# Kernel optimization log

Measured on AMD Instinct MI355X. Metric: run time of the kernel, lower is better.

The kernel has to match this reference:

```python
import jax, jax.numpy as jnp
import numpy as np

B = 512
N_ENT = 100000
N_REL = 64
D = 200          # embed_dim
D1 = 10          # embed_shape (emb_dim1)
D2 = 20          # embed_dim // embed_shape (emb_dim2)
K = 3            # kernel_size
C = 32           # out_channels
FC_IN = C * (2 * D1 - K + 1) * (D2 - K + 1)  # 32*18*18 = 10368
EPS = 1e-5       # BatchNorm eps
LS = 0.1         # label_smoothing
LAM = 1e-5       # kg_l2_loss_lambda


def setup_inputs() -> dict:
    key = jax.random.key(0)
    ks = jax.random.split(key, 8)
    return dict(
        entity_w=jax.random.normal(ks[0], (N_ENT, D), jnp.float32) * 0.1,
        relation_w=jax.random.normal(ks[1], (N_REL, D), jnp.float32) * 0.1,
        conv_w=jax.random.normal(ks[2], (C, 1, K, K), jnp.float32) * 0.1,
        conv_b=jnp.zeros((C,), jnp.float32),
        fc_w=jax.random.normal(ks[3], (D, FC_IN), jnp.float32) * 0.02,
        fc_b=jnp.zeros((D,), jnp.float32),
        b=jnp.zeros((N_ENT,), jnp.float32),
        bn0_g=jnp.ones((1,), jnp.float32), bn0_b=jnp.zeros((1,), jnp.float32),
        bn1_g=jnp.ones((C,), jnp.float32), bn1_b=jnp.zeros((C,), jnp.float32),
        bn2_g=jnp.ones((D,), jnp.float32), bn2_b=jnp.zeros((D,), jnp.float32),
        h=jax.random.randint(ks[4], (B,), 0, N_ENT),
        r=jax.random.randint(ks[5], (B,), 0, N_REL),
        pos_t=jax.random.randint(ks[6], (B,), 0, N_ENT),
    )


def _bn(x, g, b, axes, shape):
    # training-mode batchnorm (batch statistics), biased variance as in torch
    m = jnp.mean(x, axes, keepdims=True)
    v = jnp.var(x, axes, keepdims=True)
    return (x - m) * jax.lax.rsqrt(v + EPS) * g.reshape(shape) + b.reshape(shape)


def _l2_mean(x):
    # torch: mean(sum(x**2, dim=1) / 2)
    return jnp.mean(jnp.sum(x * x, axis=1) / 2.0)


def reference(entity_w, relation_w, conv_w, conv_b, fc_w, fc_b, b,
              bn0_g, bn0_b, bn1_g, bn1_b, bn2_g, bn2_b, h, r, pos_t):
    h_e = entity_w[h].reshape(B, 1, D1, D2)
    r_e = relation_w[r].reshape(B, 1, D1, D2)
    x = jnp.concatenate([h_e, r_e], axis=2)           # [B,1,2*D1,D2]
    x = _bn(x, bn0_g, bn0_b, (0, 2, 3), (1, 1, 1, 1))
    x = jax.lax.conv_general_dilated(
        x, conv_w, (1, 1), 'VALID',
        dimension_numbers=('NCHW', 'OIHW', 'NCHW')) + conv_b.reshape(1, C, 1, 1)
    x = _bn(x, bn1_g, bn1_b, (0, 2, 3), (1, C, 1, 1))
    x = jax.nn.relu(x).reshape(B, -1)                 # [B, FC_IN]
    x = x @ fc_w.T + fc_b                             # [B, D]
    x = _bn(x, bn2_g, bn2_b, (0,), (1, D))
    x = jax.nn.leaky_relu(x)                          # slope 0.01 = torch default
    scores = x @ entity_w.T + b                       # [B, N_ENT]
    # BCEWithLogits with smoothed label y = (1-LS)*onehot(pos_t) + 1/N_ENT,
    # loss = mean(softplus(s) - s*y); one-hot never materialized.
    sp_sum = jnp.sum(jax.nn.softplus(scores))
    xy_sum = jnp.sum(scores) / N_ENT + (1.0 - LS) * jnp.sum(
        scores[jnp.arange(B), pos_t])
    kg_loss = (sp_sum - xy_sum) / (B * N_ENT)
    l2 = _l2_mean(h_e) + _l2_mean(r_e) + _l2_mean(conv_w) + _l2_mean(fc_w)
    return kg_loss + LAM * l2
```

## Files before the change

### kernel.cpp

```cpp
#include <hip/hip_runtime.h>
#include <math.h>

#define NB_B 512
#define NE 100000
#define NE_PAD 100032
#define DD 200
#define CC 32
#define FCIN 10368
#define HW 324
#define BNEPS 1e-5f
#define KP 224

#define ENT_BLKS 10941
#define FCW_BLKS 1013
#define GATH_OFF (ENT_BLKS + FCW_BLKS)

typedef __attribute__((ext_vector_type(8))) short short8;
typedef __attribute__((ext_vector_type(4))) float floatx4;


static __device__ __forceinline__ float blk_reduce(float v, volatile float* sbuf) {
  for (int o = 32; o > 0; o >>= 1) v += __shfl_down(v, o, 64);
  int lane = threadIdx.x & 63, wid = threadIdx.x >> 6;
  if (lane == 0) sbuf[wid] = v;
  __syncthreads();
  float r = 0.f;
  int nw = (blockDim.x + 63) >> 6;
  if ((int)threadIdx.x < nw) r = sbuf[threadIdx.x];
  if (threadIdx.x < 64) {
    for (int o = 32; o > 0; o >>= 1) r += __shfl_down(r, o, 64);
  }
  __syncthreads();
  return r;
}

static __device__ __forceinline__ unsigned short f32_to_bf16(float f) {
  unsigned int u = __float_as_uint(f);
  u += 0x7fffu + ((u >> 16) & 1u);
  return (unsigned short)(u >> 16);
}
static __device__ __forceinline__ float bf16_to_f32(unsigned short b) {
  return __uint_as_float(((unsigned int)b) << 16);
}

__global__ __launch_bounds__(256) void k_cvt(const float* __restrict__ ent,
                                             unsigned short* __restrict__ entb,
                                             const float* __restrict__ fcw,
                                             unsigned short* __restrict__ fcwb,
                                             const float* __restrict__ rel,
                                             const int* __restrict__ h,
                                             const int* __restrict__ r,
                                             float* __restrict__ x0,
                                             double* dacc) {
  if (blockIdx.x < ENT_BLKS) {
    int g = blockIdx.x * 256 + threadIdx.x;
    int row = g / 28;
    int c8 = (g - row * 28) * 8;
    ushort4 o0, o1;
    if (c8 < 200 && row < NE) {
      const float4* s = (const float4*)(ent + (long)row * DD + c8);
      float4 u = s[0], v = s[1];
      o0.x = f32_to_bf16(u.x); o0.y = f32_to_bf16(u.y);
      o0.z = f32_to_bf16(u.z); o0.w = f32_to_bf16(u.w);
      o1.x = f32_to_bf16(v.x); o1.y = f32_to_bf16(v.y);
      o1.z = f32_to_bf16(v.z); o1.w = f32_to_bf16(v.w);
    } else {
      o0.x = o0.y = o0.z = o0.w = 0;
      o1.x = o1.y = o1.z = o1.w = 0;
    }
    ushort4* d = (ushort4*)(entb + (long)row * KP + c8);
    d[0] = o0; d[1] = o1;
  } else if (blockIdx.x < GATH_OFF) {
    int g = (blockIdx.x - ENT_BLKS) * 256 + threadIdx.x;
    float sq = 0.f;
    if (g < 259200) {
      const float4* s = (const float4*)(fcw + (long)g * 8);
      float4 u = s[0], v = s[1];
      sq = u.x*u.x + u.y*u.y + u.z*u.z + u.w*u.w
         + v.x*v.x + v.y*v.y + v.z*v.z + v.w*v.w;
      ushort4 o0, o1;
      o0.x = f32_to_bf16(u.x); o0.y = f32_to_bf16(u.y);
      o0.z = f32_to_bf16(u.z); o0.w = f32_to_bf16(u.w);
      o1.x = f32_to_bf16(v.x); o1.y = f32_to_bf16(v.y);
      o1.z = f32_to_bf16(v.z); o1.w = f32_to_bf16(v.w);
      ushort4* d = (ushort4*)(fcwb + (long)g * 8);
      d[0] = o0; d[1] = o1;
    }
    __shared__ float sbuf[8];
    float tq = blk_reduce(sq, sbuf);
    if (threadIdx.x == 0) atomicAdd(&dacc[67], (double)tq);
  } else {
    int b = blockIdx.x - GATH_OFF;
    int hi = h[b], ri = r[b];
    float s = 0.f, sq = 0.f;
    for (int i = threadIdx.x; i < 400; i += 256) {
      float v = (i < 200) ? ent[(long)hi * DD + i] : rel[(long)ri * DD + (i - 200)];
      x0[b * 400 + i] = v;
      s += v; sq += v * v;
    }
    __shared__ float sbuf[8];
    float ts = blk_reduce(s, sbuf);
    float tq = blk_reduce(sq, sbuf);
    if (threadIdx.x == 0) {
      atomicAdd(&dacc[0], (double)ts);
      atomicAdd(&dacc[1], (double)tq);
    }
  }
}

__global__ __launch_bounds__(256) void k_conv(const float* __restrict__ x0,
                       const float* __restrict__ convw, const float* __restrict__ convb,
                       const float* __restrict__ g0, const float* __restrict__ b0,
                       unsigned short* __restrict__ yb, double* dacc) {
  __shared__ float xs[400], wsm[288], cbs[32], ssum[32], ssq[32];
  __shared__ float a0s, s0s;
  int b = blockIdx.x, t = threadIdx.x;
  for (int i = t; i < 400; i += 256) xs[i] = x0[b * 400 + i];
  for (int i = t; i < 288; i += 256) wsm[i] = convw[i];
  if (t < 32) cbs[t] = convb[t];
  if (t == 0) {
    double m = dacc[0] / 204800.0;
    double v = dacc[1] / 204800.0 - m * m;
    float a = g0[0] * rsqrtf((float)v + BNEPS);
    a0s = a; s0s = b0[0] - (float)m * a;
  }
  __syncthreads();
  float a0 = a0s, s0 = s0s;
  for (int i = t; i < 400; i += 256) xs[i] = a0 * xs[i] + s0;
  __syncthreads();
  int c = t >> 3, sub = t & 7;
  const float* w = &wsm[c * 9];
  float cb = cbs[c];
  float s = 0.f, sq = 0.f;
  for (int e = sub; e < HW; e += 8) {
    int oh = e / 18, ow = e - oh * 18;
    const float* xp = &xs[oh * 20 + ow];
    float acc = cb
       + xp[0] * w[0] + xp[1] * w[1] + xp[2] * w[2]
       + xp[20] * w[3] + xp[21] * w[4] + xp[22] * w[5]
       + xp[40] * w[6] + xp[41] * w[7] + xp[42] * w[8];
    yb[(long)b * FCIN + c * HW + e] = f32_to_bf16(acc);
    s += acc; sq += acc * acc;
  }
  s += __shfl_xor(s, 1, 64); sq += __shfl_xor(sq, 1, 64);
  s += __shfl_xor(s, 2, 64); sq += __shfl_xor(sq, 2, 64);
  s += __shfl_xor(s, 4, 64); sq += __shfl_xor(sq, 4, 64);
  if (sub == 0) { ssum[c] = s; ssq[c] = sq; }
  __syncthreads();
  if (t < 32) {
    atomicAdd(&dacc[2 + t], (double)ssum[t]);
    atomicAdd(&dacc[34 + t], (double)ssq[t]);
  }
}

__global__ __launch_bounds__(256) void k_prep(unsigned short* __restrict__ yb,
                                              const float* __restrict__ g1,
                                              const float* __restrict__ b1,
                                              const double* __restrict__ dacc) {
  __shared__ float a1s[32], sh1s[32];
  int t = threadIdx.x;
  if (t < 32) {
    double cnt = 512.0 * 324.0;
    double m = dacc[2 + t] / cnt, v = dacc[34 + t] / cnt - m * m;
    float a = g1[t] * rsqrtf((float)v + BNEPS);
    a1s[t] = a; sh1s[t] = b1[t] - (float)m * a;
  }
  __syncthreads();
  int g = blockIdx.x * 256 + t;
  int row = g / 1296;
  int c8 = (g - row * 1296) * 8;
  unsigned short* p = yb + (long)row * FCIN + c8;
  ushort4 v0 = ((ushort4*)p)[0], v1 = ((ushort4*)p)[1];
  unsigned short e[8] = {v0.x, v0.y, v0.z, v0.w, v1.x, v1.y, v1.z, v1.w};
#pragma unroll
  for (int j = 0; j < 8; j++) {
    int c = (c8 + j) / HW;
    float f = a1s[c] * bf16_to_f32(e[j]) + sh1s[c];
    e[j] = f32_to_bf16(fmaxf(f, 0.f));
  }
  v0.x = e[0]; v0.y = e[1]; v0.z = e[2]; v0.w = e[3];
  v1.x = e[4]; v1.y = e[5]; v1.z = e[6]; v1.w = e[7];
  ((ushort4*)p)[0] = v0; ((ushort4*)p)[1] = v1;
}

__global__ __launch_bounds__(64) void k_fc3(const unsigned short* __restrict__ yb,
                                            const unsigned short* __restrict__ fcwb,
                                            float* __restrict__ Cp) {
  int wid = blockIdx.x;
  int ks = wid >> 5, rem = wid & 31;
  int mt = rem >> 2, nt = rem & 3;
  int m0 = mt * 64, n0 = nt * 64;
  int lane = threadIdx.x;
  int quad = lane >> 4, lr = lane & 15;
  long kbeg = (long)ks * 864;

  const unsigned short* arow[4];
  const unsigned short* brow[4];
#pragma unroll
  for (int mi = 0; mi < 4; mi++)
    arow[mi] = yb + (long)(m0 + mi * 16 + lr) * FCIN + kbeg + quad * 8;
#pragma unroll
  for (int ni = 0; ni < 4; ni++) {
    int d = n0 + ni * 16 + lr;
    if (d > DD - 1) d = DD - 1;
    brow[ni] = fcwb + (long)d * FCIN + kbeg + quad * 8;
  }

  floatx4 acc[4][4];
#pragma unroll
  for (int i = 0; i < 4; i++)
#pragma unroll
    for (int j = 0; j < 4; j++) acc[i][j] = (floatx4){0.f, 0.f, 0.f, 0.f};

  short8 sA[3][4], sB[3][4];
#pragma unroll
  for (int c = 0; c < 3; c++) {
#pragma unroll
    for (int mi = 0; mi < 4; mi++) sA[c][mi] = *(const short8*)(arow[mi] + c * 32);
#pragma unroll
    for (int ni = 0; ni < 4; ni++) sB[c][ni] = *(const short8*)(brow[ni] + c * 32);
  }
  for (int c3 = 0; c3 < 9; c3++) {
    int cc = c3 * 3;
#pragma unroll
    for (int j = 0; j < 3; j++) {
#pragma unroll
      for (int ni = 0; ni < 4; ni++)
#pragma unroll
        for (int mi = 0; mi < 4; mi++)
          acc[mi][ni] = __builtin_amdgcn_mfma_f32_16x16x32_bf16(sA[j][mi], sB[j][ni], acc[mi][ni], 0, 0, 0);
      int nxt = cc + j + 3;
      if (nxt < 27) {
#pragma unroll
        for (int mi = 0; mi < 4; mi++) sA[j][mi] = *(const short8*)(arow[mi] + nxt * 32);
#pragma unroll
        for (int ni = 0; ni < 4; ni++) sB[j][ni] = *(const short8*)(brow[ni] + nxt * 32);
      }
    }
  }

  float* out = Cp + (long)ks * (NB_B * DD);
#pragma unroll
  for (int ni = 0; ni < 4; ni++) {
    int d = n0 + ni * 16 + lr;
    if (d < DD) {
#pragma unroll
      for (int mi = 0; mi < 4; mi++) {
        int mbase = m0 + mi * 16 + quad * 4;
#pragma unroll
        for (int rg = 0; rg < 4; rg++)
          out[(mbase + rg) * DD + d] = acc[mi][ni][rg];
      }
    }
  }
}

__global__ void k_fcbn(const float* __restrict__ Cp, const float* __restrict__ fcb,
                       const float* __restrict__ g2, const float* __restrict__ b2,
                       float* __restrict__ Cfc, float* __restrict__ a2,
                       float* __restrict__ b2c) {
  int d = blockIdx.x, lane = threadIdx.x;
  float fb = fcb[d];
  float s = 0.f, sq = 0.f;
  for (int b = lane; b < NB_B; b += 64) {
    float v = 0.f;
#pragma unroll
    for (int p = 0; p < 12; p++) v += Cp[(long)p * (NB_B * DD) + b * DD + d];
    Cfc[b * DD + d] = v;
    float w = v + fb;
    s += w; sq += w * w;
  }
  for (int o = 32; o > 0; o >>= 1) { s += __shfl_down(s, o, 64); sq += __shfl_down(sq, o, 64); }
  if (lane == 0) {
    float m = s / 512.f, v = sq / 512.f - m * m;
    float a = g2[d] * rsqrtf(v + BNEPS);
    a2[d] = a; b2c[d] = b2[d] - m * a;
  }
}

__global__ __launch_bounds__(256) void k_xfinal(const float* __restrict__ Cfc,
                         const float* __restrict__ fcb,
                         const float* __restrict__ a2, const float* __restrict__ b2c,
                         const float* __restrict__ ent, const float* __restrict__ bias,
                         const int* __restrict__ pos,
                         float* __restrict__ xf, unsigned short* __restrict__ xfb,
                         double* dacc) {
  __shared__ float xs[224];
  __shared__ float sbuf[8];
  int b = blockIdx.x, t = threadIdx.x;
  if (t < KP) {
    float xv = 0.f;
    if (t < DD) {
      float v = Cfc[b * DD + t] + fcb[t];
      xv = a2[t] * v + b2c[t];
      xv = xv >= 0.f ? xv : 0.01f * xv;
      xf[b * DD + t] = xv;
    }
    xfb[b * KP + t] = f32_to_bf16(xv);
    xs[t] = xv;
  }
  __syncthreads();
  int e = pos[b];
  float s = (t < DD) ? xs[t] * ent[(long)e * DD + t] : 0.f;
  float ts = blk_reduce(s, sbuf);
  if (t == 0) atomicAdd(&dacc[70], (double)(ts + bias[e]));
}

static __device__ __forceinline__ void sc_compute8(
    const unsigned short* __restrict__ buf, const float (&bv)[2],
    const short8 (&af)[2][7], int quad, int lr, float& sp, float& ss) {
#pragma unroll
  for (int ni = 0; ni < 2; ni++) {
    float b1v = bv[ni];
    floatx4 acc0 = (floatx4){0.f, 0.f, 0.f, 0.f};
    floatx4 acc1 = (floatx4){0.f, 0.f, 0.f, 0.f};
#pragma unroll
    for (int kc = 0; kc < 7; kc++) {
      int c = kc * 4 + quad;
      short8 bsv = *(const short8*)(buf + (ni * 16 + lr) * KP + c * 8);
      acc0 = __builtin_amdgcn_mfma_f32_16x16x32_bf16(af[0][kc], bsv, acc0, 0, 0, 0);
      acc1 = __builtin_amdgcn_mfma_f32_16x16x32_bf16(af[1][kc], bsv, acc1, 0, 0, 0);
    }
#pragma unroll
    for (int rg2 = 0; rg2 < 4; rg2++) {
      float s1 = acc0[rg2] + b1v;
      ss += s1;
      float m1 = s1 * 1.4426950408889634f;
      float e2 = __builtin_amdgcn_exp2f(-__builtin_fabsf(m1));
      sp += fmaxf(m1, 0.f) + __builtin_amdgcn_logf(1.f + e2);
    }
#pragma unroll
    for (int rg2 = 0; rg2 < 4; rg2++) {
      float s1 = acc1[rg2] + b1v;
      ss += s1;
      float m1 = s1 * 1.4426950408889634f;
      float e2 = __builtin_amdgcn_exp2f(-__builtin_fabsf(m1));
      sp += fmaxf(m1, 0.f) + __builtin_amdgcn_logf(1.f + e2);
    }
  }
}

__global__ __launch_bounds__(512) void k_scores8(
    const unsigned short* __restrict__ entb,
    const unsigned short* __restrict__ xfb,
    const float* __restrict__ bias, double* dacc) {
  __shared__ unsigned short Bs[2][7168];
  __shared__ float sbuf[8];
  int t = threadIdx.x;
  int wv = t >> 6, lane = t & 63;
  int quad = lane >> 4, lr = lane & 15;
  int b = blockIdx.x;
  int rh = b & 1;
  int trip = b >> 1;
  int e0 = trip * 96;

  short8 af[2][7];
#pragma unroll
  for (int mi = 0; mi < 2; mi++) {
    const unsigned short* ap =
        xfb + (size_t)(rh * 256 + wv * 32 + mi * 16 + lr) * KP + quad * 8;
#pragma unroll
    for (int kc = 0; kc < 7; kc++) af[mi][kc] = *(const short8*)(ap + kc * 32);
  }

  float bv[3][2];
#pragma unroll
  for (int tt = 0; tt < 3; tt++)
#pragma unroll
    for (int ni = 0; ni < 2; ni++) {
      int e = e0 + tt * 32 + ni * 16 + lr;
      bv[tt][ni] = (e < NE) ? bias[e] : 0.f;
    }

#define STAGE8(bufi, tile)                                                     \
  {                                                                            \
    _Pragma("unroll")                                                          \
    for (int i_ = 0; i_ < 2; i_++) {                                           \
      int s_ = wv * 2 + i_;                                                    \
      if (s_ < 14) {                                                           \
        const unsigned short* gp_ =                                            \
            entb + (size_t)(e0 + (tile) * 32) * KP + s_ * 512 + lane * 8;      \
        __builtin_amdgcn_global_load_lds(                                      \
            (const __attribute__((address_space(1))) unsigned int*)gp_,       \
            (__attribute__((address_space(3))) unsigned int*)&Bs[bufi][s_ * 512], \
            16, 0, 0);                                                         \
      }                                                                        \
    }                                                                          \
  }

  float sp = 0.f, ss = 0.f;

  STAGE8(0, 0);
  STAGE8(1, 1);
  __syncthreads();

  sc_compute8(Bs[0], bv[0], af, quad, lr, sp, ss);
  __syncthreads();
  STAGE8(0, 2);
  sc_compute8(Bs[1], bv[1], af, quad, lr, sp, ss);
  __syncthreads();
  sc_compute8(Bs[0], bv[2], af, quad, lr, sp, ss);
#undef STAGE8

  sp *= 0.6931471805599453f;
  float tsp = blk_reduce(sp, sbuf);
  float tss = blk_reduce(ss, sbuf);
  if (t == 0) {
    atomicAdd(&dacc[68], (double)tsp);
    atomicAdd(&dacc[69], (double)tss);
  }
}

__global__ void k_final(const float* __restrict__ convw, const double* dacc, float* out) {
  int t = threadIdx.x;
  float sq = 0.f;
  for (int i = t; i < 288; i += 64) { float w = convw[i]; sq += w * w; }
  for (int o = 32; o > 0; o >>= 1) sq += __shfl_down(sq, o, 64);
  if (t == 0) {
    double SP = dacc[68] - 16384.0 * 0.6931471805599453;
    double S2 = dacc[69], S3 = dacc[70];
    double xy = S2 / (double)NE + 0.9 * S3;
    double kg = (SP - xy) / ((double)NB_B * (double)NE);
    double l2 = dacc[1] / 204800.0 + (double)sq / 576.0 + dacc[67] / 400.0;
    out[0] = (float)(kg + 1e-5 * l2);
  }
}

extern "C" void kernel_launch(void* const* d_in, const int* in_sizes, int n_in,
                              void* d_out, int out_size, void* d_ws, size_t ws_size,
                              hipStream_t stream) {
  const float* ent   = (const float*)d_in[0];
  const float* rel   = (const float*)d_in[1];
  const float* convw = (const float*)d_in[2];
  const float* convb = (const float*)d_in[3];
  const float* fcw   = (const float*)d_in[4];
  const float* fcb   = (const float*)d_in[5];
  const float* bias  = (const float*)d_in[6];
  const float* g0    = (const float*)d_in[7];
  const float* b0    = (const float*)d_in[8];
  const float* g1    = (const float*)d_in[9];
  const float* b1    = (const float*)d_in[10];
  const float* g2    = (const float*)d_in[11];
  const float* b2    = (const float*)d_in[12];
  const int*   h     = (const int*)d_in[13];
  const int*   r     = (const int*)d_in[14];
  const int*   pos   = (const int*)d_in[15];

  char* ws = (char*)d_ws;
  double* dacc = (double*)(ws + 0);
  float* a2  = (float*)(ws + 16384 + 256);
  float* b2c = (float*)(ws + 16384 + 1056);
  float* x0  = (float*)(ws + 32768);
  float* Cfc = (float*)(ws + 851968);
  float* xf  = (float*)(ws + 1261568);
  unsigned short* yb   = (unsigned short*)(ws + 1671168);
  unsigned short* fcwb = (unsigned short*)(ws + 12288000);
  unsigned short* xfb  = (unsigned short*)(ws + 16435200);
  unsigned short* entb = (unsigned short*)(ws + 16664576);
  float* Cp = (float*)(ws + 61507584);

  hipMemsetAsync(dacc, 0, 8192, stream);

  k_cvt<<<GATH_OFF + 512, 256, 0, stream>>>(ent, entb, fcw, fcwb, rel, h, r, x0, dacc);
  k_conv<<<512, 256, 0, stream>>>(x0, convw, convb, g0, b0, yb, dacc);
  k_prep<<<2592, 256, 0, stream>>>(yb, g1, b1, dacc);
  k_fc3<<<384, 64, 0, stream>>>(yb, fcwb, Cp);
  k_fcbn<<<200, 64, 0, stream>>>(Cp, fcb, g2, b2, Cfc, a2, b2c);
  k_xfinal<<<512, 256, 0, stream>>>(Cfc, fcb, a2, b2c, ent, bias, pos, xf, xfb, dacc);
  k_scores8<<<2084, 512, 0, stream>>>(entb, xfb, bias, dacc);
  k_final<<<1, 64, 0, stream>>>(convw, dacc, (float*)d_out);
}
```

Before: 321.7 us.

## Rebalance scores kernel into 1024 persistent blocks with 6-7 pipelined tiles each

The scores GEMM kernel now launches 1024 blocks, each processing 6 or 7 consecutive 32-entity tiles with a double-buffered LDS pipeline, instead of 2084 blocks of 3 tiles. This amortizes per-block A-fragment loads, bias setup and atomic reductions over more tiles, and balances work across CUs. The trade-off is longer per-block dependency chains and fewer blocks available for latency hiding.

```diff
diff --git a/kernel.cpp b/kernel.cpp
--- a/kernel.cpp
+++ b/kernel.cpp
@@ -306,7 +306,7 @@
   if (t == 0) atomicAdd(&dacc[70], (double)(ts + bias[e]));
 }
 
-static __device__ __forceinline__ void sc_compute8(
+static __device__ __forceinline__ void sc_compute9(
     const unsigned short* __restrict__ buf, const float (&bv)[2],
     const short8 (&af)[2][7], int quad, int lr, float& sp, float& ss) {
 #pragma unroll
@@ -340,7 +340,7 @@
   }
 }
 
-__global__ __launch_bounds__(512) void k_scores8(
+__global__ __launch_bounds__(512) void k_scores9(
     const unsigned short* __restrict__ entb,
     const unsigned short* __restrict__ xfb,
     const float* __restrict__ bias, double* dacc) {
@@ -351,8 +351,9 @@
   int quad = lane >> 4, lr = lane & 15;
   int b = blockIdx.x;
   int rh = b & 1;
-  int trip = b >> 1;
-  int e0 = trip * 96;
+  int chunk = b >> 1;
+  int nt = (chunk < 54) ? 7 : 6;
+  int t0 = chunk * 6 + (chunk < 54 ? chunk : 54);
 
   short8 af[2][7];
 #pragma unroll
@@ -363,23 +364,23 @@
     for (int kc = 0; kc < 7; kc++) af[mi][kc] = *(const short8*)(ap + kc * 32);
   }
 
-  float bv[3][2];
-#pragma unroll
-  for (int tt = 0; tt < 3; tt++)
+  float bv[7][2];
+#pragma unroll
+  for (int i = 0; i < 7; i++)
 #pragma unroll
     for (int ni = 0; ni < 2; ni++) {
-      int e = e0 + tt * 32 + ni * 16 + lr;
-      bv[tt][ni] = (e < NE) ? bias[e] : 0.f;
-    }
-
-#define STAGE8(bufi, tile)                                                     \
+      int e = (t0 + i) * 32 + ni * 16 + lr;
+      bv[i][ni] = (i < nt && e < NE) ? bias[e] : 0.f;
+    }
+
+#define STAGE9(bufi, tile)                                                     \
   {                                                                            \
     _Pragma("unroll")                                                          \
     for (int i_ = 0; i_ < 2; i_++) {                                           \
       int s_ = wv * 2 + i_;                                                    \
       if (s_ < 14) {                                                           \
         const unsigned short* gp_ =                                            \
-            entb + (size_t)(e0 + (tile) * 32) * KP + s_ * 512 + lane * 8;      \
+            entb + (size_t)(tile) * 32 * KP + s_ * 512 + lane * 8;             \
         __builtin_amdgcn_global_load_lds(                                      \
             (const __attribute__((address_space(1))) unsigned int*)gp_,       \
             (__attribute__((address_space(3))) unsigned int*)&Bs[bufi][s_ * 512], \
@@ -390,17 +391,17 @@
 
   float sp = 0.f, ss = 0.f;
 
-  STAGE8(0, 0);
-  STAGE8(1, 1);
-  __syncthreads();
-
-  sc_compute8(Bs[0], bv[0], af, quad, lr, sp, ss);
-  __syncthreads();
-  STAGE8(0, 2);
-  sc_compute8(Bs[1], bv[1], af, quad, lr, sp, ss);
-  __syncthreads();
-  sc_compute8(Bs[0], bv[2], af, quad, lr, sp, ss);
-#undef STAGE8
+  STAGE9(0, t0);
+  __syncthreads();
+#pragma unroll
+  for (int i = 0; i < 7; i++) {
+    if (i < nt) {
+      if (i + 1 < nt) STAGE9((i + 1) & 1, t0 + i + 1);
+      sc_compute9(Bs[i & 1], bv[i], af, quad, lr, sp, ss);
+      __syncthreads();
+    }
+  }
+#undef STAGE9
 
   sp *= 0.6931471805599453f;
   float tsp = blk_reduce(sp, sbuf);
@@ -467,6 +468,6 @@
   k_fc3<<<384, 64, 0, stream>>>(yb, fcwb, Cp);
   k_fcbn<<<200, 64, 0, stream>>>(Cp, fcb, g2, b2, Cfc, a2, b2c);
   k_xfinal<<<512, 256, 0, stream>>>(Cfc, fcb, a2, b2c, ent, bias, pos, xf, xfb, dacc);
-  k_scores8<<<2084, 512, 0, stream>>>(entb, xfb, bias, dacc);
+  k_scores9<<<1024, 512, 0, stream>>>(entb, xfb, bias, dacc);
   k_final<<<1, 64, 0, stream>>>(convw, dacc, (float*)d_out);
 }
```

Measured after the change: 370.1 us. 1.15x slower.
